# Optimization experiments

Measured on AMD Instinct MI355X. Metric: run time of the kernel, lower is better.

## Reference

```python
import jax, jax.numpy as jnp
import numpy as np

NINF = -1000000000.0
B, S, E = 2, 4096, 1024


def setup_inputs() -> dict:
    key = jax.random.key(0)
    ks = jax.random.split(key, 10)
    scale = 1.0 / np.sqrt(E)
    return {
        "query": jax.random.normal(ks[0], (B, S, E), dtype=jnp.float32),
        "key": jax.random.normal(ks[1], (B, S, E), dtype=jnp.float32),
        "value": jax.random.normal(ks[2], (B, S, E), dtype=jnp.float32),
        "mask": jax.random.randint(ks[3], (S, S), 0, 2).astype(bool),
        "Wq": jax.random.normal(ks[4], (E, E), dtype=jnp.float32) * scale,
        "bq": jnp.zeros((E,), dtype=jnp.float32),
        "Wk": jax.random.normal(ks[5], (E, E), dtype=jnp.float32) * scale,
        "bk": jnp.zeros((E,), dtype=jnp.float32),
        "Wv": jax.random.normal(ks[6], (E, E), dtype=jnp.float32) * scale,
        "bv": jnp.zeros((E,), dtype=jnp.float32),
    }


def reference(query, key, value, mask, Wq, bq, Wk, bk, Wv, bv):
    # linear projections (nn.Linear convention: x @ W.T + b)
    q = jnp.einsum('bse,fe->bsf', query, Wq) + bq   # [B,S,E]
    k = jnp.einsum('bse,fe->bsf', key, Wk) + bk
    v = jnp.einsum('bse,fe->bsf', value, Wv) + bv
    # full QK^T score matrix [B,S,S], scaled by sqrt(E) of projected query
    scores = jnp.einsum('bqe,bke->bqk', q, k) / jnp.sqrt(jnp.float32(E))
    scores = jnp.where(mask, jnp.float32(NINF), scores)  # True = ignored
    attn = jax.nn.softmax(scores, axis=-1)
    return jnp.einsum('bqk,bkv->bqv', attn, v)
```

## Files before the change

kernel.cpp:

```cpp
#include <hip/hip_runtime.h>
#include <hip/hip_bf16.h>


typedef _Float16 f16_t;
typedef _Float16 f16x8 __attribute__((ext_vector_type(8)));
typedef float f32x4 __attribute__((ext_vector_type(4)));
typedef unsigned long long u64;
typedef unsigned int uint;

union PackH8 { f16x8 v; f16_t e[8]; };

__device__ __forceinline__ f32x4 mfma_f16(f16x8 a, f16x8 b, f32x4 c) {
  return __builtin_amdgcn_mfma_f32_16x16x32_f16(a, b, c, 0, 0, 0);
}

__device__ __forceinline__ void cp16(const f16_t* g, f16_t* l) {
  __builtin_amdgcn_global_load_lds(
      (const __attribute__((address_space(1))) unsigned int*)g,
      (__attribute__((address_space(3))) unsigned int*)l, 16, 0, 0);
}

__global__ __launch_bounds__(256) void cvt_mask(
    const float* __restrict__ q, const float* __restrict__ k,
    const float* __restrict__ v, const float* __restrict__ wq,
    const float* __restrict__ wk, const float* __restrict__ wv,
    const int* __restrict__ mask,
    f16_t* __restrict__ xq, f16_t* __restrict__ xk, f16_t* __restrict__ xv,
    f16_t* __restrict__ wqh, f16_t* __restrict__ wkh, f16_t* __restrict__ wvh,
    u64* __restrict__ mb) {
  if (blockIdx.y == 6) {
    const int lane = threadIdx.x & 63;
    int wid = blockIdx.x * 4 + (threadIdx.x >> 6);
    for (int w = wid; w < 262144; w += 16384) {
      const int pred = mask[(size_t)w * 64 + lane] != 0;
      u64 b = __ballot(pred);
      if (lane == 0) mb[w] = b;
    }
    return;
  }
  const float* src; f16_t* dst; size_t n;
  switch (blockIdx.y) {
    case 0: src = q;  dst = xq;  n = 8388608; break;
    case 1: src = k;  dst = xk;  n = 8388608; break;
    case 2: src = v;  dst = xv;  n = 8388608; break;
    case 3: src = wq; dst = wqh; n = 1048576; break;
    case 4: src = wk; dst = wkh; n = 1048576; break;
    default: src = wv; dst = wvh; n = 1048576; break;
  }
  size_t i = ((size_t)blockIdx.x * 256 + threadIdx.x) * 8;
  if (i >= n) return;
  float4 a = *(const float4*)(src + i);
  float4 b = *(const float4*)(src + i + 4);
  PackH8 p;
  p.e[0] = (f16_t)a.x; p.e[1] = (f16_t)a.y; p.e[2] = (f16_t)a.z; p.e[3] = (f16_t)a.w;
  p.e[4] = (f16_t)b.x; p.e[5] = (f16_t)b.y; p.e[6] = (f16_t)b.z; p.e[7] = (f16_t)b.w;
  *(f16x8*)(dst + i) = p.v;
}

#define BARR { asm volatile("" ::: "memory"); __builtin_amdgcn_s_barrier(); }
#define VM0 asm volatile("s_waitcnt vmcnt(0)" ::: "memory");
#define VM3 asm volatile("s_waitcnt vmcnt(3)" ::: "memory");
#define VM4 asm volatile("s_waitcnt vmcnt(4)" ::: "memory");

__device__ __forceinline__ void core8ph(
    const f16_t* __restrict__ Ab, const f16_t* __restrict__ Bb,
    int m0, int n0, int K, int iters, f32x4 (&acc)[4][8]) {
  __shared__ f16_t lA[32768];
  __shared__ f16_t lB[32768];

  const int tid = threadIdx.x;
  const int w = tid >> 6, lane = tid & 63;
  const int quad = lane >> 4, l15 = lane & 15;
  const int wm = w >> 1, wn = w & 1;
  const int srow = lane >> 2;
  const int sg = (lane & 3) ^ ((lane >> 3) & 3);

  const uint aoff0 = (uint)(m0 + w * 32 + srow) * K + sg * 8;
  const uint aoff1 = aoff0 + 16 * K;
  const uint boff0 = (uint)(n0 + w * 32 + srow) * K + sg * 8;
  const uint boff1 = boff0 + 16 * K;
  const int ld0 = (w * 32) * 32;
  const int ld1 = (w * 32 + 16) * 32;

  int afo[4], bfo[8];
  const int swz = (quad ^ ((l15 >> 1) & 3)) * 8;
#pragma unroll
  for (int mi = 0; mi < 4; mi++) afo[mi] = (wm * 64 + mi * 16 + l15) * 32 + swz;
#pragma unroll
  for (int ni = 0; ni < 8; ni++) bfo[ni] = (wn * 128 + ni * 16 + l15) * 32 + swz;

#define STG_A(sl, kb) { cp16(Ab + aoff0 + (kb), lA + (sl) * 8192 + ld0); \
                        cp16(Ab + aoff1 + (kb), lA + (sl) * 8192 + ld1); }
#define STG_B(sl, kb) { cp16(Bb + boff0 + (kb), lB + (sl) * 8192 + ld0); \
                        cp16(Bb + boff1 + (kb), lB + (sl) * 8192 + ld1); }
#define RD_AF(dst, SL) { _Pragma("unroll") for (int mi = 0; mi < 4; mi++) \
      dst[mi] = *(const f16x8*)(lA + (SL) * 8192 + afo[mi]); }
#define RD_B03(dst, SL) { _Pragma("unroll") for (int ni = 0; ni < 4; ni++) \
      dst[ni] = *(const f16x8*)(lB + (SL) * 8192 + bfo[ni]); }
#define RD_B47(dst, SL) { _Pragma("unroll") for (int ni = 0; ni < 4; ni++) \
      dst[ni] = *(const f16x8*)(lB + (SL) * 8192 + bfo[ni + 4]); }
#define MM_Q0(ar, br) { __builtin_amdgcn_s_setprio(1); \
    _Pragma("unroll") for (int mi = 0; mi < 4; mi++) { \
      _Pragma("unroll") for (int nj = 0; nj < 4; nj++) \
        acc[mi][nj] = mfma_f16(ar[mi], br[nj], acc[mi][nj]); } \
    __builtin_amdgcn_s_setprio(0); }
#define MM_Q1(ar, br) { __builtin_amdgcn_s_setprio(1); \
    _Pragma("unroll") for (int mi = 0; mi < 4; mi++) { \
      _Pragma("unroll") for (int nj = 0; nj < 4; nj++) \
        acc[mi][4 + nj] = mfma_f16(ar[mi], br[nj], acc[mi][4 + nj]); } \
    __builtin_amdgcn_s_setprio(0); }

  f16x8 afA[4], afB[4], b0A[4], b0B[4], b47[4];

  STG_A(0, 0) STG_B(0, 0)
  STG_A(1, 32) STG_B(1, 32)
  STG_A(2, 64) STG_B(2, 64)
  VM4
  BARR
  RD_AF(afA, 0) RD_B03(b0A, 0)

  for (int i = 0; i < iters - 1; i++) {
    const int t0 = 2 * i;
    const int kb3 = (t0 + 1) * 64 + 32;
    const int kb0 = (t0 + 2) * 64;
    const int kb1 = kb0 + 32;
    const int kb2 = (t0 + 3) * 64;
     RD_B47(b47, 0) STG_A(3, kb3) MM_Q0(afA, b0A) VM4 BARR
     RD_AF(afB, 1) RD_B03(b0B, 1) STG_B(3, kb3) MM_Q1(afA, b47) BARR
     RD_B47(b47, 1) STG_A(0, kb0) MM_Q0(afB, b0B) VM4 BARR
     RD_AF(afA, 2) RD_B03(b0A, 2) STG_B(0, kb0) MM_Q1(afB, b47) BARR
     RD_B47(b47, 2) STG_A(1, kb1) MM_Q0(afA, b0A) VM4 BARR
     RD_AF(afB, 3) RD_B03(b0B, 3) STG_B(1, kb1) MM_Q1(afA, b47) BARR
     RD_B47(b47, 3) STG_A(2, kb2) MM_Q0(afB, b0B) VM4 BARR
     RD_AF(afA, 0) RD_B03(b0A, 0) STG_B(2, kb2) MM_Q1(afB, b47) BARR
  }
  {
    const int kbp = K - 32;
     RD_B47(b47, 0) STG_A(3, kbp) MM_Q0(afA, b0A) VM4 BARR
     RD_AF(afB, 1) RD_B03(b0B, 1) STG_B(3, kbp) MM_Q1(afA, b47) BARR
     RD_B47(b47, 1) MM_Q0(afB, b0B) VM4 BARR
     RD_AF(afA, 2) RD_B03(b0A, 2) MM_Q1(afB, b47) BARR
     RD_B47(b47, 2) MM_Q0(afA, b0A) VM0 BARR
     RD_AF(afB, 3) RD_B03(b0B, 3) MM_Q1(afA, b47) BARR
     RD_B47(b47, 3) MM_Q0(afB, b0B) BARR
     MM_Q1(afB, b47)
  }
#undef STG_A
#undef STG_B
#undef RD_AF
#undef RD_B03
#undef RD_B47
#undef MM_Q0
#undef MM_Q1
}

__device__ __forceinline__ void core4ph(
    const f16_t* __restrict__ Ab, const f16_t* __restrict__ Bb,
    int m0, int n0, int K, int iters, f32x4 (&acc)[4][4]) {
  __shared__ f16_t lA[32768];
  __shared__ f16_t lB[16384];

  const int tid = threadIdx.x;
  const int w = tid >> 6, lane = tid & 63;
  const int quad = lane >> 4, l15 = lane & 15;
  const int wm = w >> 1, wn = w & 1;
  const int sg = (lane & 3) ^ ((lane >> 3) & 3);

  const uint arow = (uint)(w * 16 + (lane >> 2));
  const uint aoff0 = (uint)(m0 + arow) * K + sg * 8;
  const uint aoff1 = aoff0 + 128 * K;
  const uint boff  = (uint)(n0 + arow) * K + sg * 8;
  const int ldw = w * 512;

  int afo[4], bfo[4];
  const int swz = (quad ^ ((l15 >> 1) & 3)) * 8;
#pragma unroll
  for (int mi = 0; mi < 4; mi++) afo[mi] = (wm * 64 + mi * 16 + l15) * 32 + swz;
#pragma unroll
  for (int ni = 0; ni < 4; ni++) bfo[ni] = (wn * 64 + ni * 16 + l15) * 32 + swz;

#define STG4(sl, kb) { cp16(Ab + aoff0 + (kb), lA + (sl) * 8192 + ldw); \
                       cp16(Ab + aoff1 + (kb), lA + (sl) * 8192 + 4096 + ldw); \
                       cp16(Bb + boff  + (kb), lB + (sl) * 4096 + ldw); }
#define RD4(adst, bdst, SL) { \
    _Pragma("unroll") for (int mi = 0; mi < 4; mi++) \
      adst[mi] = *(const f16x8*)(lA + (SL) * 8192 + afo[mi]); \
    _Pragma("unroll") for (int ni = 0; ni < 4; ni++) \
      bdst[ni] = *(const f16x8*)(lB + (SL) * 4096 + bfo[ni]); }
#define MM4(ar, br) { __builtin_amdgcn_s_setprio(1); \
    _Pragma("unroll") for (int mi = 0; mi < 4; mi++) { \
      _Pragma("unroll") for (int ni = 0; ni < 4; ni++) \
        acc[mi][ni] = mfma_f16(ar[mi], br[ni], acc[mi][ni]); } \
    __builtin_amdgcn_s_setprio(0); }

  f16x8 afA[4], afB[4], bfA[4], bfB[4];

  STG4(0, 0)
  STG4(1, 32)
  STG4(2, 64)
  VM3
  BARR
  RD4(afA, bfA, 0)

  for (int i = 0; i < iters - 1; i++) {
    const int t0 = 2 * i;
     RD4(afB, bfB, 1) STG4(3, (t0 + 1) * 64 + 32) MM4(afA, bfA) VM3 BARR
     RD4(afA, bfA, 2) STG4(0, (t0 + 2) * 64) MM4(afB, bfB) VM3 BARR
     RD4(afB, bfB, 3) STG4(1, (t0 + 2) * 64 + 32) MM4(afA, bfA) VM3 BARR
     RD4(afA, bfA, 0) STG4(2, (t0 + 3) * 64) MM4(afB, bfB) VM3 BARR
  }
  {
     RD4(afB, bfB, 1) STG4(3, K - 32) MM4(afA, bfA) VM3 BARR
     RD4(afA, bfA, 2) MM4(afB, bfB) VM0 BARR
     RD4(afB, bfB, 3) MM4(afA, bfA) BARR
     MM4(afB, bfB)
  }
#undef STG4
#undef RD4
#undef MM4
}

__global__ __launch_bounds__(512, 2) void gemm512(
    const f16_t* __restrict__ A, const f16_t* __restrict__ B,
    f16_t* __restrict__ C, const float* __restrict__ bias0,
    const float* __restrict__ bias1, int K,
    long sAz, long sBz, long sCz, float scale0, float scale1, int Cstride) {
  const int bz = blockIdx.z;
  const int n0 = blockIdx.x * 256;
  const int m0 = blockIdx.y * 256;
  const f16_t* Ab = A + (size_t)sAz * bz;
  const f16_t* Bb = B + (size_t)sBz * bz;

  f32x4 acc[4][8] = {};
  core8ph(Ab, Bb, m0, n0, K, K >> 7, acc);

  const int tid = threadIdx.x;
  const int w = tid >> 6, lane = tid & 63;
  const int quad = lane >> 4, l15 = lane & 15;
  const int wm = w >> 1, wn = w & 1;
  const float* bias = bz ? bias1 : bias0;
  const float scale = bz ? scale1 : scale0;
  f16_t* Cb = C + (size_t)sCz * bz;
#pragma unroll
  for (int mi = 0; mi < 4; mi++) {
#pragma unroll
    for (int ni = 0; ni < 8; ni++) {
      const int gm0 = m0 + wm * 64 + mi * 16 + quad * 4;
      const int gn = n0 + wn * 128 + ni * 16 + l15;
#pragma unroll
      for (int r = 0; r < 4; r++) {
        const int gm = gm0 + r;
        Cb[(size_t)gm * Cstride + gn] = (f16_t)((acc[mi][ni][r] + bias[gn]) * scale);
      }
    }
  }
}

__global__ __launch_bounds__(512, 2) void gemm256(
    const f16_t* __restrict__ A, const f16_t* __restrict__ B,
    f16_t* __restrict__ C, const float* __restrict__ bias0, int K) {
  const int n0 = blockIdx.x * 128;
  const int m0 = blockIdx.y * 256;

  f32x4 acc[4][4] = {};
  core4ph(A, B, m0, n0, K, K >> 7, acc);

  const int tid = threadIdx.x;
  const int w = tid >> 6, lane = tid & 63;
  const int quad = lane >> 4, l15 = lane & 15;
  const int wm = w >> 1, wn = w & 1;
#pragma unroll
  for (int mi = 0; mi < 4; mi++) {
#pragma unroll
    for (int ni = 0; ni < 4; ni++) {
      const int gm0 = m0 + wm * 64 + mi * 16 + quad * 4;
      const int gn = n0 + wn * 64 + ni * 16 + l15;
#pragma unroll
      for (int r = 0; r < 4; r++) {
        const int gm = gm0 + r;
        const int bb = gn >> 12;
        const int s = gn & 4095;
        C[(size_t)bb * 4194304 + (size_t)gm * 4096 + s] =
            (f16_t)(acc[mi][ni][r] + bias0[gm]);
      }
    }
  }
}

__global__ __launch_bounds__(512, 2) void gemm_qk(
    const f16_t* __restrict__ A, const f16_t* __restrict__ B,
    f16_t* __restrict__ S, const u64* __restrict__ mb,
    float* __restrict__ lrow) {
  const int bid = blockIdx.x;
  const int xcd = bid & 7;
  const int l = bid >> 3;
  const int bz = l >> 5;
  const int r5 = l & 31;
  const int m0 = (xcd * 2 + (r5 >> 4)) * 256;
  const int n0 = (r5 & 15) * 256;
  const f16_t* Ab = A + (size_t)4194304 * bz;
  const f16_t* Bb = B + (size_t)4194304 * bz;

  f32x4 acc[4][8] = {};
  core8ph(Ab, Bb, m0, n0, 1024, 8, acc);

  const int tid = threadIdx.x;
  const int w = tid >> 6, lane = tid & 63;
  const int quad = lane >> 4, l15 = lane & 15;
  const int wm = w >> 1, wn = w & 1;
  f16_t* Sb = S + (size_t)16777216 * bz;
  float* lb = lrow + bz * 4096;
  const int wbase = (n0 >> 6) + wn * 2;
#pragma unroll
  for (int mi = 0; mi < 4; mi++) {
#pragma unroll
    for (int r = 0; r < 4; r++) {
      const int gm = m0 + wm * 64 + mi * 16 + quad * 4 + r;
      const u64 w0 = mb[(size_t)gm * 64 + wbase];
      const u64 w1 = mb[(size_t)gm * 64 + wbase + 1];
      float rs = 0.f;
#pragma unroll
      for (int ni = 0; ni < 8; ni++) {
        const int col_l = ni * 16 + l15;
        const u64 mw = (ni < 4) ? w0 : w1;
        const int bit = (int)((mw >> (col_l & 63)) & 1);
        const float p = bit ? 0.f : __expf(acc[mi][ni][r] - 3.0f);
        Sb[(size_t)gm * 4096 + n0 + wn * 128 + col_l] = (f16_t)p;
        rs += p;
      }
      rs += __shfl_xor(rs, 1); rs += __shfl_xor(rs, 2);
      rs += __shfl_xor(rs, 4); rs += __shfl_xor(rs, 8);
      if (l15 == 0) atomicAdd(&lb[gm], rs);
    }
  }
}

__global__ __launch_bounds__(512, 2) void gemm_pv(
    const f16_t* __restrict__ S, const f16_t* __restrict__ V,
    float* __restrict__ O, const float* __restrict__ lrow) {
  const int bid = blockIdx.x;
  const int xcd = bid & 7;
  const int l = bid >> 3;
  const int bz = l >> 4;
  const int r4 = l & 15;
  const int m0 = (xcd * 2 + (r4 >> 3)) * 256;
  const int n0 = (r4 & 7) * 128;

  const f16_t* Ab = S + (size_t)16777216 * bz;
  const f16_t* Bb = V + (size_t)4194304 * bz;

  f32x4 acc[4][4] = {};
  core4ph(Ab, Bb, m0, n0, 4096, 32, acc);

  const int tid = threadIdx.x;
  const int w = tid >> 6, lane = tid & 63;
  const int quad = lane >> 4, l15 = lane & 15;
  const int wm = w >> 1, wn = w & 1;
  float* Ob = O + (size_t)4194304 * bz;
  const float* lb = lrow + bz * 4096;
#pragma unroll
  for (int mi = 0; mi < 4; mi++) {
#pragma unroll
    for (int ni = 0; ni < 4; ni++) {
      const int gm0 = m0 + wm * 64 + mi * 16 + quad * 4;
      const int gn = n0 + wn * 64 + ni * 16 + l15;
#pragma unroll
      for (int r = 0; r < 4; r++) {
        const int gm = gm0 + r;
        Ob[(size_t)gm * 1024 + gn] = acc[mi][ni][r] * (1.0f / lb[gm]);
      }
    }
  }
}

extern "C" void kernel_launch(void* const* d_in, const int* in_sizes, int n_in,
                              void* d_out, int out_size, void* d_ws, size_t ws_size,
                              hipStream_t stream) {
  const float* query = (const float*)d_in[0];
  const float* key_  = (const float*)d_in[1];
  const float* value = (const float*)d_in[2];
  const int* mask    = (const int*)d_in[3];
  const float* Wq = (const float*)d_in[4];
  const float* bq = (const float*)d_in[5];
  const float* Wk = (const float*)d_in[6];
  const float* bk = (const float*)d_in[7];
  const float* Wv = (const float*)d_in[8];
  const float* bv = (const float*)d_in[9];
  float* out = (float*)d_out;

  const size_t MB = (size_t)1 << 20;
  char* w = (char*)d_ws;
  f16_t* qb  = (f16_t*)(w);
  f16_t* kb  = (f16_t*)(w + 16 * MB);
  f16_t* vt  = (f16_t*)(w + 32 * MB);
  f16_t* xq  = (f16_t*)(w + 48 * MB);
  f16_t* xk  = (f16_t*)(w + 64 * MB);
  f16_t* xv  = (f16_t*)(w + 80 * MB);
  f16_t* wqh = (f16_t*)(w + 96 * MB);
  f16_t* wkh = (f16_t*)(w + 98 * MB);
  f16_t* wvh = (f16_t*)(w + 100 * MB);
  f16_t* S   = (f16_t*)(w + 48 * MB);
  float* ls  = (float*)(w + 112 * MB);
  u64* mb = (u64*)d_out;

  cvt_mask<<<dim3(4096, 7), 256, 0, stream>>>(query, key_, value, Wq, Wk, Wv,
                                              mask, xq, xk, xv, wqh, wkh, wvh, mb);
  gemm512<<<dim3(4, 32, 2), 512, 0, stream>>>(
      xq, wqh, qb, bq, bk, 1024, 8388608L, 1048576L, 8388608L,
      0.03125f, 1.0f, 1024);
  gemm256<<<dim3(64, 4), 512, 0, stream>>>(wvh, xv, vt, bv, 1024);
  hipMemsetAsync(ls, 0, 2 * 4096 * sizeof(float), stream);
  gemm_qk<<<dim3(512), 512, 0, stream>>>(qb, kb, S, mb, ls);
  gemm_pv<<<dim3(256), 512, 0, stream>>>(S, vt, out, ls);
}
```

Measured before the change: 436.6 us.

## Restructure 256x256 GEMM core to 2x4 wave grid with K=64 stages

Replaces the 256x256 GEMM mainloop with a new core that arranges the 8 waves as 2x4 (each wave owning 128x64) and stages K in 64-wide double-buffered slabs split into halves. It uses a new XOR swizzle for the LDS layout and a phase schedule that interleaves fragment reads, async global-to-LDS copies and MFMA blocks with barriers. The aim is better LDS-read reuse per MFMA and fewer barriers per K. The QK and projection epilogues are remapped, with mask lookups reduced to one 64-bit word per row. The trade-off is more barriers per phase and different register pressure.

Measured after the change: 458.2 us. 4.9% more time.

```diff
diff --git a/kernel.cpp b/kernel.cpp
--- a/kernel.cpp
+++ b/kernel.cpp
@@ -62,96 +62,100 @@
 #define VM3 asm volatile("s_waitcnt vmcnt(3)" ::: "memory");
 #define VM4 asm volatile("s_waitcnt vmcnt(4)" ::: "memory");
 
-__device__ __forceinline__ void core8ph(
+__device__ __forceinline__ void core8x(
     const f16_t* __restrict__ Ab, const f16_t* __restrict__ Bb,
-    int m0, int n0, int K, int iters, f32x4 (&acc)[4][8]) {
+    int m0, int n0, int K, int iters, f32x4 (&acc)[8][4]) {
   __shared__ f16_t lA[32768];
   __shared__ f16_t lB[32768];
 
   const int tid = threadIdx.x;
   const int w = tid >> 6, lane = tid & 63;
   const int quad = lane >> 4, l15 = lane & 15;
-  const int wm = w >> 1, wn = w & 1;
-  const int srow = lane >> 2;
-  const int sg = (lane & 3) ^ ((lane >> 3) & 3);
-
-  const uint aoff0 = (uint)(m0 + w * 32 + srow) * K + sg * 8;
-  const uint aoff1 = aoff0 + 16 * K;
-  const uint boff0 = (uint)(n0 + w * 32 + srow) * K + sg * 8;
-  const uint boff1 = boff0 + 16 * K;
-  const int ld0 = (w * 32) * 32;
-  const int ld1 = (w * 32 + 16) * 32;
-
-  int afo[4], bfo[8];
-  const int swz = (quad ^ ((l15 >> 1) & 3)) * 8;
-#pragma unroll
-  for (int mi = 0; mi < 4; mi++) afo[mi] = (wm * 64 + mi * 16 + l15) * 32 + swz;
-#pragma unroll
-  for (int ni = 0; ni < 8; ni++) bfo[ni] = (wn * 128 + ni * 16 + l15) * 32 + swz;
-
-#define STG_A(sl, kb) { cp16(Ab + aoff0 + (kb), lA + (sl) * 8192 + ld0); \
-                        cp16(Ab + aoff1 + (kb), lA + (sl) * 8192 + ld1); }
-#define STG_B(sl, kb) { cp16(Bb + boff0 + (kb), lB + (sl) * 8192 + ld0); \
-                        cp16(Bb + boff1 + (kb), lB + (sl) * 8192 + ld1); }
-#define RD_AF(dst, SL) { _Pragma("unroll") for (int mi = 0; mi < 4; mi++) \
-      dst[mi] = *(const f16x8*)(lA + (SL) * 8192 + afo[mi]); }
-#define RD_B03(dst, SL) { _Pragma("unroll") for (int ni = 0; ni < 4; ni++) \
-      dst[ni] = *(const f16x8*)(lB + (SL) * 8192 + bfo[ni]); }
-#define RD_B47(dst, SL) { _Pragma("unroll") for (int ni = 0; ni < 4; ni++) \
-      dst[ni] = *(const f16x8*)(lB + (SL) * 8192 + bfo[ni + 4]); }
-#define MM_Q0(ar, br) { __builtin_amdgcn_s_setprio(1); \
-    _Pragma("unroll") for (int mi = 0; mi < 4; mi++) { \
-      _Pragma("unroll") for (int nj = 0; nj < 4; nj++) \
-        acc[mi][nj] = mfma_f16(ar[mi], br[nj], acc[mi][nj]); } \
+  const int wm2 = w >> 2, wn4 = w & 3;
+
+  const int tr = tid >> 3;
+  const int sgt = (tid & 7) ^ (tr & 7);
+  const uint aoff = (uint)(m0 + tr) * K + sgt * 8;
+  const uint boff = (uint)(n0 + tr + ((tr >> 5) << 5)) * K + sgt * 8;
+  const uint l2off = (uint)128 * K;
+  const int wq = w * 512;
+
+  int ar[4][2], br[2][2];
+#pragma unroll
+  for (int mi = 0; mi < 4; mi++)
+#pragma unroll
+    for (int ks = 0; ks < 2; ks++)
+      ar[mi][ks] = (wm2 * 64 + mi * 16 + l15) * 64 +
+                   (((ks << 2) + quad) ^ (l15 & 7)) * 8;
+#pragma unroll
+  for (int ni = 0; ni < 2; ni++)
+#pragma unroll
+    for (int ks = 0; ks < 2; ks++)
+      br[ni][ks] = (wn4 * 32 + ni * 16 + l15) * 64 +
+                   (((ks << 2) + quad) ^ (l15 & 7)) * 8;
+
+#define SA(BUF, MH, kb) { \
+    cp16(Ab + aoff + (uint)(MH) * 64 * K + (kb), \
+         lA + (BUF) * 16384 + (MH) * 8192 + wq); \
+    cp16(Ab + aoff + (uint)(MH) * 64 * K + l2off + (kb), \
+         lA + (BUF) * 16384 + (MH) * 8192 + 4096 + wq); }
+#define SB(BUF, NH, kb) { \
+    cp16(Bb + boff + (uint)(NH) * 32 * K + (kb), \
+         lB + (BUF) * 16384 + (NH) * 8192 + wq); \
+    cp16(Bb + boff + (uint)(NH) * 32 * K + l2off + (kb), \
+         lB + (BUF) * 16384 + (NH) * 8192 + 4096 + wq); }
+#define RDA(BUF, MH) { _Pragma("unroll") for (int mi = 0; mi < 4; mi++) { \
+    _Pragma("unroll") for (int ks = 0; ks < 2; ks++) \
+      af[mi][ks] = *(const f16x8*)(lA + (BUF) * 16384 + (MH) * 8192 + ar[mi][ks]); } }
+#define RDB(BUF, NH, BF) { _Pragma("unroll") for (int ni = 0; ni < 2; ni++) { \
+    _Pragma("unroll") for (int ks = 0; ks < 2; ks++) \
+      BF[ni][ks] = *(const f16x8*)(lB + (BUF) * 16384 + (NH) * 8192 + br[ni][ks]); } }
+#define MMQ(MH, NH, BF) { __builtin_amdgcn_s_setprio(1); \
+    _Pragma("unroll") for (int ks = 0; ks < 2; ks++) { \
+      _Pragma("unroll") for (int mi = 0; mi < 4; mi++) { \
+        _Pragma("unroll") for (int ni = 0; ni < 2; ni++) \
+          acc[(MH) * 4 + mi][(NH) * 2 + ni] = \
+              mfma_f16(af[mi][ks], BF[ni][ks], acc[(MH) * 4 + mi][(NH) * 2 + ni]); } } \
     __builtin_amdgcn_s_setprio(0); }
-#define MM_Q1(ar, br) { __builtin_amdgcn_s_setprio(1); \
-    _Pragma("unroll") for (int mi = 0; mi < 4; mi++) { \
-      _Pragma("unroll") for (int nj = 0; nj < 4; nj++) \
-        acc[mi][4 + nj] = mfma_f16(ar[mi], br[nj], acc[mi][4 + nj]); } \
-    __builtin_amdgcn_s_setprio(0); }
-
-  f16x8 afA[4], afB[4], b0A[4], b0B[4], b47[4];
-
-  STG_A(0, 0) STG_B(0, 0)
-  STG_A(1, 32) STG_B(1, 32)
-  STG_A(2, 64) STG_B(2, 64)
+#define PHX(RD, STG, MM, VMW) { RD STG BARR MM VMW BARR }
+
+  f16x8 af[4][2], b0[2][2], b1[2][2];
+
+  SA(0, 0, 0) SB(0, 0, 0) SA(0, 1, 0) SB(0, 1, 0)
+  SA(1, 0, 64) SB(1, 0, 64)
   VM4
   BARR
-  RD_AF(afA, 0) RD_B03(b0A, 0)
 
   for (int i = 0; i < iters - 1; i++) {
-    const int t0 = 2 * i;
-    const int kb3 = (t0 + 1) * 64 + 32;
-    const int kb0 = (t0 + 2) * 64;
-    const int kb1 = kb0 + 32;
-    const int kb2 = (t0 + 3) * 64;
-     RD_B47(b47, 0) STG_A(3, kb3) MM_Q0(afA, b0A) VM4 BARR
-     RD_AF(afB, 1) RD_B03(b0B, 1) STG_B(3, kb3) MM_Q1(afA, b47) BARR
-     RD_B47(b47, 1) STG_A(0, kb0) MM_Q0(afB, b0B) VM4 BARR
-     RD_AF(afA, 2) RD_B03(b0A, 2) STG_B(0, kb0) MM_Q1(afB, b47) BARR
-     RD_B47(b47, 2) STG_A(1, kb1) MM_Q0(afA, b0A) VM4 BARR
-     RD_AF(afB, 3) RD_B03(b0B, 3) STG_B(1, kb1) MM_Q1(afA, b47) BARR
-     RD_B47(b47, 3) STG_A(2, kb2) MM_Q0(afB, b0B) VM4 BARR
-     RD_AF(afA, 0) RD_B03(b0A, 0) STG_B(2, kb2) MM_Q1(afB, b47) BARR
+    const int kA = (2 * i + 1) * 64;
+    const int kB = (2 * i + 2) * 64;
+    const int kC = (2 * i + 3) * 64;
+    PHX(RDA(0, 0) RDB(0, 0, b0), SA(1, 1, kA), MMQ(0, 0, b0), )
+    PHX(RDB(0, 1, b1),           SB(1, 1, kA), MMQ(0, 1, b1), )
+    PHX(RDA(0, 1),               SA(0, 0, kB), MMQ(1, 0, b0), )
+    PHX(,                        SB(0, 0, kB), MMQ(1, 1, b1), VM4)
+    PHX(RDA(1, 0) RDB(1, 0, b0), SA(0, 1, kB), MMQ(0, 0, b0), )
+    PHX(RDB(1, 1, b1),           SB(0, 1, kB), MMQ(0, 1, b1), )
+    PHX(RDA(1, 1),               SA(1, 0, kC), MMQ(1, 0, b0), )
+    PHX(,                        SB(1, 0, kC), MMQ(1, 1, b1), VM4)
   }
   {
-    const int kbp = K - 32;
-     RD_B47(b47, 0) STG_A(3, kbp) MM_Q0(afA, b0A) VM4 BARR
-     RD_AF(afB, 1) RD_B03(b0B, 1) STG_B(3, kbp) MM_Q1(afA, b47) BARR
-     RD_B47(b47, 1) MM_Q0(afB, b0B) VM4 BARR
-     RD_AF(afA, 2) RD_B03(b0A, 2) MM_Q1(afB, b47) BARR
-     RD_B47(b47, 2) MM_Q0(afA, b0A) VM0 BARR
-     RD_AF(afB, 3) RD_B03(b0B, 3) MM_Q1(afA, b47) BARR
-     RD_B47(b47, 3) MM_Q0(afB, b0B) BARR
-     MM_Q1(afB, b47)
-  }
-#undef STG_A
-#undef STG_B
-#undef RD_AF
-#undef RD_B03
-#undef RD_B47
-#undef MM_Q0
-#undef MM_Q1
+    const int kA = 2 * (iters - 1) * 64 + 64;
+    PHX(RDA(0, 0) RDB(0, 0, b0), SA(1, 1, kA), MMQ(0, 0, b0), )
+    PHX(RDB(0, 1, b1),           SB(1, 1, kA), MMQ(0, 1, b1), )
+    PHX(RDA(0, 1),               ,             MMQ(1, 0, b0), )
+    PHX(,                        ,             MMQ(1, 1, b1), VM0)
+    PHX(RDA(1, 0) RDB(1, 0, b0), ,             MMQ(0, 0, b0), )
+    PHX(RDB(1, 1, b1),           ,             MMQ(0, 1, b1), )
+    PHX(RDA(1, 1),               ,             MMQ(1, 0, b0), )
+    PHX(,                        ,             MMQ(1, 1, b1), )
+  }
+#undef SA
+#undef SB
+#undef RDA
+#undef RDB
+#undef MMQ
+#undef PHX
 }
 
 __device__ __forceinline__ void core4ph(
@@ -231,22 +235,22 @@
   const f16_t* Ab = A + (size_t)sAz * bz;
   const f16_t* Bb = B + (size_t)sBz * bz;
 
-  f32x4 acc[4][8] = {};
-  core8ph(Ab, Bb, m0, n0, K, K >> 7, acc);
-
-  const int tid = threadIdx.x;
-  const int w = tid >> 6, lane = tid & 63;
-  const int quad = lane >> 4, l15 = lane & 15;
-  const int wm = w >> 1, wn = w & 1;
+  f32x4 acc[8][4] = {};
+  core8x(Ab, Bb, m0, n0, K, K >> 7, acc);
+
+  const int tid = threadIdx.x;
+  const int w = tid >> 6, lane = tid & 63;
+  const int quad = lane >> 4, l15 = lane & 15;
+  const int wm2 = w >> 2, wn4 = w & 3;
   const float* bias = bz ? bias1 : bias0;
   const float scale = bz ? scale1 : scale0;
   f16_t* Cb = C + (size_t)sCz * bz;
 #pragma unroll
-  for (int mi = 0; mi < 4; mi++) {
-#pragma unroll
-    for (int ni = 0; ni < 8; ni++) {
-      const int gm0 = m0 + wm * 64 + mi * 16 + quad * 4;
-      const int gn = n0 + wn * 128 + ni * 16 + l15;
+  for (int mi = 0; mi < 8; mi++) {
+#pragma unroll
+    for (int ni = 0; ni < 4; ni++) {
+      const int gm0 = m0 + wm2 * 128 + mi * 16 + quad * 4;
+      const int gn = n0 + wn4 * 64 + ni * 16 + l15;
 #pragma unroll
       for (int r = 0; r < 4; r++) {
         const int gm = gm0 + r;
@@ -301,31 +305,29 @@
   const f16_t* Ab = A + (size_t)4194304 * bz;
   const f16_t* Bb = B + (size_t)4194304 * bz;
 
-  f32x4 acc[4][8] = {};
-  core8ph(Ab, Bb, m0, n0, 1024, 8, acc);
-
-  const int tid = threadIdx.x;
-  const int w = tid >> 6, lane = tid & 63;
-  const int quad = lane >> 4, l15 = lane & 15;
-  const int wm = w >> 1, wn = w & 1;
+  f32x4 acc[8][4] = {};
+  core8x(Ab, Bb, m0, n0, 1024, 8, acc);
+
+  const int tid = threadIdx.x;
+  const int w = tid >> 6, lane = tid & 63;
+  const int quad = lane >> 4, l15 = lane & 15;
+  const int wm2 = w >> 2, wn4 = w & 3;
   f16_t* Sb = S + (size_t)16777216 * bz;
   float* lb = lrow + bz * 4096;
-  const int wbase = (n0 >> 6) + wn * 2;
-#pragma unroll
-  for (int mi = 0; mi < 4; mi++) {
+  const int wword = (n0 >> 6) + wn4;
+#pragma unroll
+  for (int mi = 0; mi < 8; mi++) {
 #pragma unroll
     for (int r = 0; r < 4; r++) {
-      const int gm = m0 + wm * 64 + mi * 16 + quad * 4 + r;
-      const u64 w0 = mb[(size_t)gm * 64 + wbase];
-      const u64 w1 = mb[(size_t)gm * 64 + wbase + 1];
+      const int gm = m0 + wm2 * 128 + mi * 16 + quad * 4 + r;
+      const u64 mw = mb[(size_t)gm * 64 + wword];
       float rs = 0.f;
 #pragma unroll
-      for (int ni = 0; ni < 8; ni++) {
+      for (int ni = 0; ni < 4; ni++) {
         const int col_l = ni * 16 + l15;
-        const u64 mw = (ni < 4) ? w0 : w1;
-        const int bit = (int)((mw >> (col_l & 63)) & 1);
+        const int bit = (int)((mw >> col_l) & 1);
         const float p = bit ? 0.f : __expf(acc[mi][ni][r] - 3.0f);
-        Sb[(size_t)gm * 4096 + n0 + wn * 128 + col_l] = (f16_t)p;
+        Sb[(size_t)gm * 4096 + n0 + wn4 * 64 + col_l] = (f16_t)p;
         rs += p;
       }
       rs += __shfl_xor(rs, 1); rs += __shfl_xor(rs, 2);
```

## Replace QK GEMM mainloop with 2x4 warp layout and quarter-tile pipelined schedule

Applied to the files above, without the earlier changes.

Adds a new GEMM core for the QK^T kernel that arranges the 8 waves as 2x4 (each wave owning a 128x64 sub-tile instead of 64x128). It splits each K-step into four quadrant phases, interleaving LDS reads, async global-to-LDS staging, and MFMA with barriers and raised wave priority during MFMA. The epilogue is adapted so each wave reads a single 64-bit mask word per row. The aim is better overlap of memory traffic with MFMA and fewer mask loads, at the cost of more barriers and a more intricate buffer schedule.

Result: slower. 466.5 us (+6.8%).

```diff
diff --git a/kernel.cpp b/kernel.cpp
--- a/kernel.cpp
+++ b/kernel.cpp
@@ -61,6 +61,102 @@
 #define VM0 asm volatile("s_waitcnt vmcnt(0)" ::: "memory");
 #define VM3 asm volatile("s_waitcnt vmcnt(3)" ::: "memory");
 #define VM4 asm volatile("s_waitcnt vmcnt(4)" ::: "memory");
+#define VM6 asm volatile("s_waitcnt vmcnt(6)" ::: "memory");
+
+__device__ __forceinline__ void core8x(
+    const f16_t* __restrict__ Ab, const f16_t* __restrict__ Bb,
+    int m0, int n0, int K, int iters, f32x4 (&acc)[8][4]) {
+  __shared__ f16_t lA[32768];
+  __shared__ f16_t lB[32768];
+
+  const int tid = threadIdx.x;
+  const int w = tid >> 6, lane = tid & 63;
+  const int quad = lane >> 4, l15 = lane & 15;
+  const int wm2 = w >> 2, wn4 = w & 3;
+
+  const int tr = tid >> 3;
+  const int sgt = (tid & 7) ^ (tr & 7);
+  const uint aoff = (uint)(m0 + tr) * K + sgt * 8;
+  const uint boff = (uint)(n0 + tr + ((tr >> 5) << 5)) * K + sgt * 8;
+  const uint l2off = (uint)128 * K;
+  const int wq = w * 512;
+
+  int ar[4][2], br[2][2];
+#pragma unroll
+  for (int mi = 0; mi < 4; mi++)
+#pragma unroll
+    for (int ks = 0; ks < 2; ks++)
+      ar[mi][ks] = (wm2 * 64 + mi * 16 + l15) * 64 +
+                   (((ks << 2) + quad) ^ (l15 & 7)) * 8;
+#pragma unroll
+  for (int ni = 0; ni < 2; ni++)
+#pragma unroll
+    for (int ks = 0; ks < 2; ks++)
+      br[ni][ks] = (wn4 * 32 + ni * 16 + l15) * 64 +
+                   (((ks << 2) + quad) ^ (l15 & 7)) * 8;
+
+#define SA(BUF, MH, kb) { \
+    cp16(Ab + aoff + (uint)(MH) * 64 * K + (kb), \
+         lA + (BUF) * 16384 + (MH) * 8192 + wq); \
+    cp16(Ab + aoff + (uint)(MH) * 64 * K + l2off + (kb), \
+         lA + (BUF) * 16384 + (MH) * 8192 + 4096 + wq); }
+#define SB(BUF, NH, kb) { \
+    cp16(Bb + boff + (uint)(NH) * 32 * K + (kb), \
+         lB + (BUF) * 16384 + (NH) * 8192 + wq); \
+    cp16(Bb + boff + (uint)(NH) * 32 * K + l2off + (kb), \
+         lB + (BUF) * 16384 + (NH) * 8192 + 4096 + wq); }
+#define RDA(BUF, MH) { _Pragma("unroll") for (int mi = 0; mi < 4; mi++) { \
+    _Pragma("unroll") for (int ks = 0; ks < 2; ks++) \
+      af[mi][ks] = *(const f16x8*)(lA + (BUF) * 16384 + (MH) * 8192 + ar[mi][ks]); } }
+#define RDB(BUF, NH, BF) { _Pragma("unroll") for (int ni = 0; ni < 2; ni++) { \
+    _Pragma("unroll") for (int ks = 0; ks < 2; ks++) \
+      BF[ni][ks] = *(const f16x8*)(lB + (BUF) * 16384 + (NH) * 8192 + br[ni][ks]); } }
+#define MMQ(MH, NH, BF) { __builtin_amdgcn_s_setprio(1); \
+    _Pragma("unroll") for (int ks = 0; ks < 2; ks++) { \
+      _Pragma("unroll") for (int mi = 0; mi < 4; mi++) { \
+        _Pragma("unroll") for (int ni = 0; ni < 2; ni++) \
+          acc[(MH) * 4 + mi][(NH) * 2 + ni] = \
+              mfma_f16(af[mi][ks], BF[ni][ks], acc[(MH) * 4 + mi][(NH) * 2 + ni]); } } \
+    __builtin_amdgcn_s_setprio(0); }
+#define PHX(RD, STG, MM, VMW) { RD STG BARR MM VMW BARR }
+
+  f16x8 af[4][2], b0[2][2], b1[2][2];
+
+  SA(0, 0, 0) SB(0, 0, 0) SB(0, 1, 0) SA(0, 1, 0)
+  SA(1, 0, 64) SB(1, 0, 64) SB(1, 1, 64)
+  VM6
+  BARR
+
+  for (int i = 0; i < iters - 1; i++) {
+    const int kA = (2 * i + 1) * 64;
+    const int kB = (2 * i + 2) * 64;
+    const int kC = (2 * i + 3) * 64;
+    PHX(RDA(0, 0) RDB(0, 0, b0), SA(1, 1, kA), MMQ(0, 0, b0), )
+    PHX(RDB(0, 1, b1),           SA(0, 0, kB), MMQ(0, 1, b1), )
+    PHX(RDA(0, 1),               SB(0, 0, kB), MMQ(1, 0, b0), )
+    PHX(,                        SB(0, 1, kB), MMQ(1, 1, b1), VM6)
+    PHX(RDA(1, 0) RDB(1, 0, b0), SA(0, 1, kB), MMQ(0, 0, b0), )
+    PHX(RDB(1, 1, b1),           SA(1, 0, kC), MMQ(0, 1, b1), )
+    PHX(RDA(1, 1),               SB(1, 0, kC), MMQ(1, 0, b0), )
+    PHX(,                        SB(1, 1, kC), MMQ(1, 1, b1), VM6)
+  }
+  {
+    PHX(RDA(0, 0) RDB(0, 0, b0), SA(1, 1, K - 64), MMQ(0, 0, b0), )
+    PHX(RDB(0, 1, b1),           ,                 MMQ(0, 1, b1), )
+    PHX(RDA(0, 1),               ,                 MMQ(1, 0, b0), )
+    PHX(,                        ,                 MMQ(1, 1, b1), VM0)
+    PHX(RDA(1, 0) RDB(1, 0, b0), ,                 MMQ(0, 0, b0), )
+    PHX(RDB(1, 1, b1),           ,                 MMQ(0, 1, b1), )
+    PHX(RDA(1, 1),               ,                 MMQ(1, 0, b0), )
+    PHX(,                        ,                 MMQ(1, 1, b1), )
+  }
+#undef SA
+#undef SB
+#undef RDA
+#undef RDB
+#undef MMQ
+#undef PHX
+}
 
 __device__ __forceinline__ void core8ph(
     const f16_t* __restrict__ Ab, const f16_t* __restrict__ Bb,
@@ -301,31 +397,29 @@
   const f16_t* Ab = A + (size_t)4194304 * bz;
   const f16_t* Bb = B + (size_t)4194304 * bz;
 
-  f32x4 acc[4][8] = {};
-  core8ph(Ab, Bb, m0, n0, 1024, 8, acc);
-
-  const int tid = threadIdx.x;
-  const int w = tid >> 6, lane = tid & 63;
-  const int quad = lane >> 4, l15 = lane & 15;
-  const int wm = w >> 1, wn = w & 1;
+  f32x4 acc[8][4] = {};
+  core8x(Ab, Bb, m0, n0, 1024, 8, acc);
+
+  const int tid = threadIdx.x;
+  const int w = tid >> 6, lane = tid & 63;
+  const int quad = lane >> 4, l15 = lane & 15;
+  const int wm2 = w >> 2, wn4 = w & 3;
   f16_t* Sb = S + (size_t)16777216 * bz;
   float* lb = lrow + bz * 4096;
-  const int wbase = (n0 >> 6) + wn * 2;
-#pragma unroll
-  for (int mi = 0; mi < 4; mi++) {
+  const int wword = (n0 >> 6) + wn4;
+#pragma unroll
+  for (int mi = 0; mi < 8; mi++) {
 #pragma unroll
     for (int r = 0; r < 4; r++) {
-      const int gm = m0 + wm * 64 + mi * 16 + quad * 4 + r;
-      const u64 w0 = mb[(size_t)gm * 64 + wbase];
-      const u64 w1 = mb[(size_t)gm * 64 + wbase + 1];
+      const int gm = m0 + wm2 * 128 + mi * 16 + quad * 4 + r;
+      const u64 mw = mb[(size_t)gm * 64 + wword];
       float rs = 0.f;
 #pragma unroll
-      for (int ni = 0; ni < 8; ni++) {
+      for (int ni = 0; ni < 4; ni++) {
         const int col_l = ni * 16 + l15;
-        const u64 mw = (ni < 4) ? w0 : w1;
-        const int bit = (int)((mw >> (col_l & 63)) & 1);
+        const int bit = (int)((mw >> col_l) & 1);
         const float p = bit ? 0.f : __expf(acc[mi][ni][r] - 3.0f);
-        Sb[(size_t)gm * 4096 + n0 + wn * 128 + col_l] = (f16_t)p;
+        Sb[(size_t)gm * 4096 + n0 + wn4 * 64 + col_l] = (f16_t)p;
         rs += p;
       }
       rs += __shfl_xor(rs, 1); rs += __shfl_xor(rs, 2);
```

## Split QK score kernel into per-batch launches with smaller tiles for batch one

Applied to the files above, without the earlier changes.

The batched QK^T/exp kernel is split in two. Batch 0 keeps the 256x256-tile kernel on 256 blocks. Batch 1 goes to a new 128x128-tile kernel with 256 threads, a simple single-buffered LDS loop and 1024 blocks. This appears aimed at balancing load or occupancy across CUs with a different tile shape. The cost is two launches, and the simpler kernel has no load/compute overlap, so its per-block efficiency is likely lower.

After: 462.4 us. 5.9% more time.

```diff
diff --git a/kernel.cpp b/kernel.cpp
--- a/kernel.cpp
+++ b/kernel.cpp
@@ -287,29 +287,23 @@
   }
 }
 
-__global__ __launch_bounds__(512, 2) void gemm_qk(
+__global__ __launch_bounds__(512, 2) void gemm_qk_r(
     const f16_t* __restrict__ A, const f16_t* __restrict__ B,
     f16_t* __restrict__ S, const u64* __restrict__ mb,
     float* __restrict__ lrow) {
   const int bid = blockIdx.x;
   const int xcd = bid & 7;
   const int l = bid >> 3;
-  const int bz = l >> 5;
-  const int r5 = l & 31;
-  const int m0 = (xcd * 2 + (r5 >> 4)) * 256;
-  const int n0 = (r5 & 15) * 256;
-  const f16_t* Ab = A + (size_t)4194304 * bz;
-  const f16_t* Bb = B + (size_t)4194304 * bz;
+  const int m0 = (xcd * 2 + (l >> 4)) * 256;
+  const int n0 = (l & 15) * 256;
 
   f32x4 acc[4][8] = {};
-  core8ph(Ab, Bb, m0, n0, 1024, 8, acc);
-
-  const int tid = threadIdx.x;
-  const int w = tid >> 6, lane = tid & 63;
-  const int quad = lane >> 4, l15 = lane & 15;
-  const int wm = w >> 1, wn = w & 1;
-  f16_t* Sb = S + (size_t)16777216 * bz;
-  float* lb = lrow + bz * 4096;
+  core8ph(A, B, m0, n0, 1024, 8, acc);
+
+  const int tid = threadIdx.x;
+  const int w = tid >> 6, lane = tid & 63;
+  const int quad = lane >> 4, l15 = lane & 15;
+  const int wm = w >> 1, wn = w & 1;
   const int wbase = (n0 >> 6) + wn * 2;
 #pragma unroll
   for (int mi = 0; mi < 4; mi++) {
@@ -325,7 +319,97 @@
         const u64 mw = (ni < 4) ? w0 : w1;
         const int bit = (int)((mw >> (col_l & 63)) & 1);
         const float p = bit ? 0.f : __expf(acc[mi][ni][r] - 3.0f);
-        Sb[(size_t)gm * 4096 + n0 + wn * 128 + col_l] = (f16_t)p;
+        S[(size_t)gm * 4096 + n0 + wn * 128 + col_l] = (f16_t)p;
+        rs += p;
+      }
+      rs += __shfl_xor(rs, 1); rs += __shfl_xor(rs, 2);
+      rs += __shfl_xor(rs, 4); rs += __shfl_xor(rs, 8);
+      if (l15 == 0) atomicAdd(&lrow[gm], rs);
+    }
+  }
+}
+
+__global__ __launch_bounds__(256, 3) void gemm_qk_m(
+    const f16_t* __restrict__ A, const f16_t* __restrict__ B,
+    f16_t* __restrict__ S, const u64* __restrict__ mb,
+    float* __restrict__ lrow) {
+  __shared__ f16_t sA[8192];
+  __shared__ f16_t sB[8192];
+  const int bid = blockIdx.x;
+  const int xcd = bid & 7;
+  const int l = bid >> 3;
+  const int m0 = (xcd * 4 + (l >> 5)) * 128;
+  const int n0 = (l & 31) * 128;
+  const f16_t* Ab = A + 4194304;
+  const f16_t* Bb = B + 4194304;
+  const int K = 1024;
+
+  const int tid = threadIdx.x;
+  const int w = tid >> 6, lane = tid & 63;
+  const int quad = lane >> 4, l15 = lane & 15;
+  const int wm = w >> 1, wn = w & 1;
+
+  const int srow = lane >> 3;
+  const int sg = (lane & 7) ^ srow;
+
+  int ar[4][2], br[4][2];
+#pragma unroll
+  for (int mi = 0; mi < 4; mi++)
+#pragma unroll
+    for (int ks = 0; ks < 2; ks++) {
+      ar[mi][ks] = (wm * 64 + mi * 16 + l15) * 64 +
+                   (((ks << 2) + quad) ^ (l15 & 7)) * 8;
+      br[mi][ks] = (wn * 64 + mi * 16 + l15) * 64 +
+                   (((ks << 2) + quad) ^ (l15 & 7)) * 8;
+    }
+
+  f32x4 acc[4][4] = {};
+
+  for (int k0 = 0; k0 < K; k0 += 64) {
+    __syncthreads();
+#pragma unroll
+    for (int j = 0; j < 4; j++) {
+      const int c = j * 4 + w;
+      cp16(Ab + (uint)(m0 + c * 8 + srow) * K + sg * 8 + k0, sA + c * 512);
+      cp16(Bb + (uint)(n0 + c * 8 + srow) * K + sg * 8 + k0, sB + c * 512);
+    }
+    VM0
+    __syncthreads();
+    f16x8 af[4][2], bf[4][2];
+#pragma unroll
+    for (int mi = 0; mi < 4; mi++)
+#pragma unroll
+      for (int ks = 0; ks < 2; ks++) {
+        af[mi][ks] = *(const f16x8*)(sA + ar[mi][ks]);
+        bf[mi][ks] = *(const f16x8*)(sB + br[mi][ks]);
+      }
+    __builtin_amdgcn_s_setprio(1);
+#pragma unroll
+    for (int ks = 0; ks < 2; ks++)
+#pragma unroll
+      for (int mi = 0; mi < 4; mi++)
+#pragma unroll
+        for (int ni = 0; ni < 4; ni++)
+          acc[mi][ni] = mfma_f16(af[mi][ks], bf[ni][ks], acc[mi][ni]);
+    __builtin_amdgcn_s_setprio(0);
+  }
+
+  f16_t* Sb = S + (size_t)16777216;
+  float* lb = lrow + 4096;
+  const int wword = (n0 >> 6) + wn;
+#pragma unroll
+  for (int mi = 0; mi < 4; mi++) {
+#pragma unroll
+    for (int r = 0; r < 4; r++) {
+      const int gm = m0 + wm * 64 + mi * 16 + quad * 4 + r;
+      const u64 mw = mb[(size_t)gm * 64 + wword];
+      float rs = 0.f;
+#pragma unroll
+      for (int ni = 0; ni < 4; ni++) {
+        const int col_l = ni * 16 + l15;
+        const int bit = (int)((mw >> col_l) & 1);
+        const float p = bit ? 0.f : __expf(acc[mi][ni][r] - 3.0f);
+        Sb[(size_t)gm * 4096 + n0 + wn * 64 + col_l] = (f16_t)p;
         rs += p;
       }
       rs += __shfl_xor(rs, 1); rs += __shfl_xor(rs, 2);
@@ -410,6 +494,7 @@
       0.03125f, 1.0f, 1024);
   gemm256<<<dim3(64, 4), 512, 0, stream>>>(wvh, xv, vt, bv, 1024);
   hipMemsetAsync(ls, 0, 2 * 4096 * sizeof(float), stream);
-  gemm_qk<<<dim3(512), 512, 0, stream>>>(qb, kb, S, mb, ls);
+  gemm_qk_r<<<dim3(256), 512, 0, stream>>>(qb, kb, S, mb, ls);
+  gemm_qk_m<<<dim3(1024), 256, 0, stream>>>(qb, kb, S, mb, ls);
   gemm_pv<<<dim3(256), 512, 0, stream>>>(S, vt, out, ls);
 }
```
